# Optimization experiments

Measured on AMD Instinct MI355X. Metric: run time of the kernel, lower is better.

The kernel has to match this reference:

```python
import jax, jax.numpy as jnp
import numpy as np

N_NODES = 100000
N_EDGES = 3200000
D_IN = 96      # sum(latent_dim)
D_OUT = 32     # latent_dim[-1]
N_HEADS = 4
LEAKY_SLOPE = 0.2


def setup_inputs() -> dict:
    key = jax.random.key(0)
    k_x, k_w, k_a, k_src, k_dst = jax.random.split(key, 5)
    x = jax.random.normal(k_x, (N_NODES, D_IN), dtype=jnp.float32)
    # per-head GAT params (xavier-ish scale)
    W = jax.random.normal(k_w, (N_HEADS, D_IN, D_OUT), dtype=jnp.float32) * (1.414 / np.sqrt(D_IN))
    a = jax.random.normal(k_a, (N_HEADS, 2 * D_OUT), dtype=jnp.float32) * 0.1
    edge_src = jax.random.randint(k_src, (N_EDGES,), 0, N_NODES)
    edge_dst = jax.random.randint(k_dst, (N_EDGES,), 0, N_NODES)
    return {"x": x, "W": W, "a": a, "edge_src": edge_src, "edge_dst": edge_dst}


def reference(x, W, a, edge_src, edge_dst):
    # Multi-head sparse GAT layer (SpGraphAttentionLayer, concat=True, eval mode).
    N = x.shape[0]
    n_heads, _, d_out = W.shape
    outs = []
    for i in range(n_heads):  # small fixed head loop; data dims fully vectorized
        h = x @ W[i]                                   # [N, d_out]
        # a @ cat(h[src], h[dst]) == h[src]@a1 + h[dst]@a2 (avoids [E, 2*d_out] concat)
        s = h[edge_src] @ a[i, :d_out] + h[edge_dst] @ a[i, d_out:]   # [E]
        edge_e = jnp.exp(-jax.nn.leaky_relu(s, LEAKY_SLOPE))          # [E]
        # sparse_coo(edge, edge_e, [N,N]) @ h  ==  scatter-add of edge_e * h[dst] into src
        msg = edge_e[:, None] * h[edge_dst]                           # [E, d_out]
        h_prime = jax.ops.segment_sum(msg, edge_src, num_segments=N)  # [N, d_out]
        outs.append(jax.nn.elu(h_prime))
    return jnp.concatenate(outs, axis=1)  # [N, n_heads * d_out]
```

## Files before the change

kernel.cpp:

```cpp
#include <hip/hip_runtime.h>
#include <hip/hip_bf16.h>

#define DIN 96
#define DOUT 32
#define NH 4
#define DTOT 128
#define SLOPE 0.2f
#define NPB 16
#define BSH 7
#define BNODES 128
#define MAXB 1024
#define EPB 16384

__device__ __forceinline__ unsigned int packbf2(float lo, float hi) {
    unsigned int a = __float_as_uint(lo), b = __float_as_uint(hi);
    a += 0x7fffu + ((a >> 16) & 1u);
    b += 0x7fffu + ((b >> 16) & 1u);
    return (a >> 16) | (b & 0xffff0000u);
}

__global__ __launch_bounds__(256) void feat_kernel(
    const float* __restrict__ x, const float* __restrict__ W,
    const float* __restrict__ a,
    unsigned int* __restrict__ hq,
    float2* __restrict__ usrc, float2* __restrict__ vdst,
    int n_nodes)
{
    __shared__ float Wl[DIN * DTOT];
    __shared__ float xs[NPB * DIN];
    __shared__ float al[NH * 2 * DOUT];
    const int t = threadIdx.x;

    for (int i = t; i < DIN * DTOT; i += 256) {
        int k = i >> 7, c = i & 127;
        int head = c >> 5, j = c & 31;
        Wl[i] = W[head * (DIN * DOUT) + k * DOUT + j];
    }
    for (int i = t; i < NH * 2 * DOUT; i += 256) al[i] = a[i];

    const int node0 = blockIdx.x * NPB;
    for (int i = t; i < NPB * DIN; i += 256) {
        int gidx = node0 * DIN + i;
        xs[i] = (gidx < n_nodes * DIN) ? x[gidx] : 0.f;
    }
    __syncthreads();

    const int node = t >> 4;
    const int cb = (t & 15) << 3;
    float acc[8];
#pragma unroll
    for (int j = 0; j < 8; ++j) acc[j] = 0.f;

#pragma unroll 4
    for (int k = 0; k < DIN; ++k) {
        float xv = xs[node * DIN + k];
#pragma unroll
        for (int j = 0; j < 8; ++j)
            acc[j] += xv * Wl[k * DTOT + cb + j];
    }

    const int g = node0 + node;
    if (g < n_nodes) {
        uint4 pk;
        pk.x = packbf2(acc[0], acc[1]);
        pk.y = packbf2(acc[2], acc[3]);
        pk.z = packbf2(acc[4], acc[5]);
        pk.w = packbf2(acc[6], acc[7]);
        *(uint4*)&hq[(size_t)g * 64 + (cb >> 1)] = pk;
    }

    const int head = cb >> 5;
    const int j0 = cb & 31;
    float ps = 0.f, pd = 0.f;
#pragma unroll
    for (int j = 0; j < 8; ++j) {
        ps += acc[j] * al[head * 64 + j0 + j];
        pd += acc[j] * al[head * 64 + 32 + j0 + j];
    }
    ps += __shfl_xor(ps, 1); ps += __shfl_xor(ps, 2);
    pd += __shfl_xor(pd, 1); pd += __shfl_xor(pd, 2);
    if ((t & 3) == 0 && g < n_nodes) {
        usrc[g * NH + head] = make_float2(__expf(-ps), __expf(-SLOPE * ps));
        vdst[g * NH + head] = make_float2(__expf(-pd), __expf(-SLOPE * pd));
    }
}


__global__ __launch_bounds__(256) void bincount_kernel(
    const int* __restrict__ esrc, int* __restrict__ counts, int n_edges, int nb)
{
    __shared__ int bc[MAXB];
    const int t = threadIdx.x;
    for (int i = t; i < nb; i += 256) bc[i] = 0;
    __syncthreads();
    const int base = blockIdx.x * EPB;
    const int end = min(base + EPB, n_edges);
    for (int e = base + t; e < end; e += 256)
        atomicAdd(&bc[esrc[e] >> BSH], 1);
    __syncthreads();
    for (int i = t; i < nb; i += 256)
        if (bc[i] > 0) atomicAdd(&counts[i], bc[i]);
}

__global__ __launch_bounds__(1024) void bscan_kernel(
    const int* __restrict__ counts, int* __restrict__ bbase,
    int* __restrict__ gcur, int* __restrict__ sbase, int nb)
{
    __shared__ int tmp[1024];
    const int t = threadIdx.x;
    int v = (t < nb) ? counts[t] : 0;
    tmp[t] = v;
    __syncthreads();
    for (int off = 1; off < 1024; off <<= 1) {
        int xv = (t >= off) ? tmp[t - off] : 0;
        __syncthreads();
        tmp[t] += xv;
        __syncthreads();
    }
    if (t < nb) {
        int excl = tmp[t] - v;
        bbase[t] = excl;
        gcur[t] = excl;
        sbase[t] = ((excl + 3) & ~3) + t * (4 * BNODES);
    }
}

__global__ __launch_bounds__(256) void binscatter_kernel(
    const int* __restrict__ esrc, const int* __restrict__ edst,
    int* __restrict__ gcur, unsigned int* __restrict__ binned,
    int n_edges, int nb)
{
    __shared__ int bc[MAXB];
    const int t = threadIdx.x;
    for (int i = t; i < nb; i += 256) bc[i] = 0;
    __syncthreads();
    const int base = blockIdx.x * EPB;
    const int end = min(base + EPB, n_edges);
    for (int e = base + t; e < end; e += 256)
        atomicAdd(&bc[esrc[e] >> BSH], 1);
    __syncthreads();
    for (int i = t; i < nb; i += 256) {
        int c = bc[i];
        bc[i] = (c > 0) ? atomicAdd(&gcur[i], c) : 0;
    }
    __syncthreads();
    for (int e = base + t; e < end; e += 256) {
        int s = esrc[e];
        int pos = atomicAdd(&bc[s >> BSH], 1);
        binned[pos] = ((unsigned int)(s & (BNODES - 1)) << 17) | (unsigned int)edst[e];
    }
}

__global__ __launch_bounds__(256) void binfine_kernel(
    const unsigned int* __restrict__ binned,
    const int* __restrict__ counts, const int* __restrict__ bbase,
    const int* __restrict__ sbase,
    int* __restrict__ offs, int* __restrict__ deg,
    int* __restrict__ slots, int n_nodes)
{
    __shared__ int dcnt[BNODES];
    __shared__ int sc[BNODES];
    __shared__ int dcur[BNODES];
    const int t = threadIdx.x;
    const int b = blockIdx.x;
    const int cnt = counts[b];
    const int start = bbase[b];
    const int sb = sbase[b];
    const int node0 = b << BSH;

    if (t < BNODES) dcnt[t] = 0;
    __syncthreads();
    for (int i = t; i < cnt; i += 256)
        atomicAdd(&dcnt[binned[start + i] >> 17], 1);
    __syncthreads();
    int pd = 0;
    if (t < BNODES) { pd = (dcnt[t] + 3) & ~3; sc[t] = pd; }
    __syncthreads();
    for (int off = 1; off < BNODES; off <<= 1) {
        int v = 0;
        if (t < BNODES && t >= off) v = sc[t - off];
        __syncthreads();
        if (t < BNODES) sc[t] += v;
        __syncthreads();
    }
    if (t < BNODES) {
        int o = sb + sc[t] - pd;
        dcur[t] = o;
        int node = node0 + t;
        if (node < n_nodes) { offs[node] = o; deg[node] = dcnt[t]; }
    }
    __syncthreads();
    for (int i = t; i < cnt; i += 256) {
        unsigned int w = binned[start + i];
        int pos = atomicAdd(&dcur[w >> 17], 1);
        slots[pos] = (int)(w & 0x1ffffu);
    }
}

__global__ __launch_bounds__(256) void gather_kernel(
    const int* __restrict__ slots, const int* __restrict__ offsets,
    const int* __restrict__ deg,
    const unsigned int* __restrict__ hv,
    const float2* __restrict__ usrc, const float2* __restrict__ vdst,
    float* __restrict__ out, int n_nodes)
{
    const int t = threadIdx.x;
    const int node = blockIdx.x * 4 + (t >> 6);
    if (node >= n_nodes) return;
    const int l = t & 63;
    const int head = l >> 4;
    const unsigned loff = (unsigned)l << 2;
    const unsigned hoff = (unsigned)head << 3;
    const char* __restrict__ hvb = (const char*)hv;
    const char* __restrict__ vdb = (const char*)vdst;
    const float2 u = usrc[(unsigned)node * 4u + head];
    const int beg = offsets[node];
    const int d = deg[node];

    float ax0 = 0.f, ay0 = 0.f, ax1 = 0.f, ay1 = 0.f;
    float ax2 = 0.f, ay2 = 0.f, ax3 = 0.f, ay3 = 0.f;

#define LDV(c) (*(const float2*)(vdb + ((((unsigned)(c)) << 5) + hoff)))
#define LDW(c) (*(const unsigned int*)(hvb + ((((unsigned)(c)) << 8) + loff)))
#define COMP(vv, ww, AX, AY) do {                                   \
        float e_ = fminf(u.x * (vv).x, u.y * (vv).y);               \
        AX = fmaf(e_, __uint_as_float((ww) << 16), AX);             \
        AY = fmaf(e_, __uint_as_float((ww) & 0xffff0000u), AY);     \
    } while (0)

    int k = 0;
    if (d >= 4) {
        int4 cA = *(const int4*)(slots + beg);
        float2 vA0 = LDV(cA.x), vA1 = LDV(cA.y), vA2 = LDV(cA.z), vA3 = LDV(cA.w);
        unsigned wA0 = LDW(cA.x), wA1 = LDW(cA.y), wA2 = LDW(cA.z), wA3 = LDW(cA.w);

        for (; k + 12 <= d; k += 8) {
            int4 cB = *(const int4*)(slots + beg + k + 4);
            float2 vB0 = LDV(cB.x), vB1 = LDV(cB.y), vB2 = LDV(cB.z), vB3 = LDV(cB.w);
            unsigned wB0 = LDW(cB.x), wB1 = LDW(cB.y), wB2 = LDW(cB.z), wB3 = LDW(cB.w);
            COMP(vA0, wA0, ax0, ay0); COMP(vA1, wA1, ax1, ay1);
            COMP(vA2, wA2, ax2, ay2); COMP(vA3, wA3, ax3, ay3);
            int4 cN = *(const int4*)(slots + beg + k + 8);
            vA0 = LDV(cN.x); vA1 = LDV(cN.y); vA2 = LDV(cN.z); vA3 = LDV(cN.w);
            wA0 = LDW(cN.x); wA1 = LDW(cN.y); wA2 = LDW(cN.z); wA3 = LDW(cN.w);
            COMP(vB0, wB0, ax0, ay0); COMP(vB1, wB1, ax1, ay1);
            COMP(vB2, wB2, ax2, ay2); COMP(vB3, wB3, ax3, ay3);
        }
        if (k + 8 <= d) {
            int4 cB = *(const int4*)(slots + beg + k + 4);
            float2 vB0 = LDV(cB.x), vB1 = LDV(cB.y), vB2 = LDV(cB.z), vB3 = LDV(cB.w);
            unsigned wB0 = LDW(cB.x), wB1 = LDW(cB.y), wB2 = LDW(cB.z), wB3 = LDW(cB.w);
            COMP(vA0, wA0, ax0, ay0); COMP(vA1, wA1, ax1, ay1);
            COMP(vA2, wA2, ax2, ay2); COMP(vA3, wA3, ax3, ay3);
            COMP(vB0, wB0, ax0, ay0); COMP(vB1, wB1, ax1, ay1);
            COMP(vB2, wB2, ax2, ay2); COMP(vB3, wB3, ax3, ay3);
            k += 8;
        } else {
            COMP(vA0, wA0, ax0, ay0); COMP(vA1, wA1, ax1, ay1);
            COMP(vA2, wA2, ax2, ay2); COMP(vA3, wA3, ax3, ay3);
            k += 4;
        }
    }
    for (; k < d; ++k) {
        int c = slots[beg + k];
        float2 v = LDV(c);
        unsigned w = LDW(c);
        COMP(v, w, ax0, ay0);
    }
#undef LDV
#undef LDW
#undef COMP

    float rx = (ax0 + ax1) + (ax2 + ax3);
    float ry = (ay0 + ay1) + (ay2 + ay3);
    rx = rx > 0.f ? rx : __expf(rx) - 1.f;
    ry = ry > 0.f ? ry : __expf(ry) - 1.f;
    ((float2*)out)[(unsigned)node * 64u + l] = make_float2(rx, ry);
}

extern "C" void kernel_launch(void* const* d_in, const int* in_sizes, int n_in,
                              void* d_out, int out_size, void* d_ws, size_t ws_size,
                              hipStream_t stream)
{
    const float* x  = (const float*)d_in[0];
    const float* W  = (const float*)d_in[1];
    const float* a  = (const float*)d_in[2];
    const int* esrc = (const int*)d_in[3];
    const int* edst = (const int*)d_in[4];
    const int n_nodes = in_sizes[0] / DIN;
    const int n_edges = in_sizes[3];
    float* out = (float*)d_out;

    const int nb = (n_nodes + BNODES - 1) >> BSH;

    unsigned int* hq = (unsigned int*)d_ws;
    float2* usrc = (float2*)(hq + (size_t)n_nodes * 64);
    float2* vdst = usrc + (size_t)n_nodes * NH;
    int* offs   = (int*)(vdst + (size_t)n_nodes * NH);
    int* deg    = offs + n_nodes;
    int* counts = deg + n_nodes;
    int* bbase  = counts + MAXB;
    int* gcur   = bbase + MAXB;
    int* sbase  = gcur + MAXB;
    unsigned int* binned = (unsigned int*)(sbase + MAXB);
    int* slots  = (int*)(binned + n_edges);

    hipMemsetAsync(counts, 0, MAXB * sizeof(int), stream);

    feat_kernel<<<(n_nodes + NPB - 1) / NPB, 256, 0, stream>>>(
        x, W, a, hq, usrc, vdst, n_nodes);

    const int binblocks = (n_edges + EPB - 1) / EPB;
    bincount_kernel<<<binblocks, 256, 0, stream>>>(esrc, counts, n_edges, nb);
    bscan_kernel<<<1, 1024, 0, stream>>>(counts, bbase, gcur, sbase, nb);
    binscatter_kernel<<<binblocks, 256, 0, stream>>>(
        esrc, edst, gcur, binned, n_edges, nb);
    binfine_kernel<<<nb, 256, 0, stream>>>(
        binned, counts, bbase, sbase, offs, deg, slots, n_nodes);

    gather_kernel<<<(n_nodes + 3) / 4, 256, 0, stream>>>(
        slots, offs, deg, hq, usrc, vdst, out, n_nodes);
}
```

Before: 501.0 us.

## Register-tile feature GEMM over four nodes and fold counts memset into it

The feature kernel now computes four nodes per thread with 64 nodes per block, reading x directly from global memory as float4 and W from shared memory as split float4 halves. This amortises the per-block W staging over more nodes and cuts shared-memory traffic per FMA. The separate memset of the bin counts is removed; block 0 of the feature kernel zeroes them instead, saving one launch. In exchange each thread holds more registers, and the grid has a quarter as many blocks.

```diff
diff --git a/kernel.cpp b/kernel.cpp
--- a/kernel.cpp
+++ b/kernel.cpp
@@ -6,7 +6,7 @@
 #define NH 4
 #define DTOT 128
 #define SLOPE 0.2f
-#define NPB 16
+#define NPBF 64
 #define BSH 7
 #define BNODES 128
 #define MAXB 1024
@@ -24,64 +24,97 @@
     const float* __restrict__ a,
     unsigned int* __restrict__ hq,
     float2* __restrict__ usrc, float2* __restrict__ vdst,
-    int n_nodes)
-{
-    __shared__ float Wl[DIN * DTOT];
-    __shared__ float xs[NPB * DIN];
+    int* __restrict__ counts, int n_nodes)
+{
+    __shared__ float Wlo[DIN * 64];
+    __shared__ float Whi[DIN * 64];
     __shared__ float al[NH * 2 * DOUT];
     const int t = threadIdx.x;
+
+    if (blockIdx.x == 0)
+        for (int i = t; i < MAXB; i += 256) counts[i] = 0;
 
     for (int i = t; i < DIN * DTOT; i += 256) {
         int k = i >> 7, c = i & 127;
         int head = c >> 5, j = c & 31;
-        Wl[i] = W[head * (DIN * DOUT) + k * DOUT + j];
+        float w = W[head * (DIN * DOUT) + k * DOUT + j];
+        int cbi = c >> 3, jj = c & 7;
+        if (jj < 4) Wlo[(k << 6) + (cbi << 2) + jj] = w;
+        else        Whi[(k << 6) + (cbi << 2) + (jj - 4)] = w;
     }
     for (int i = t; i < NH * 2 * DOUT; i += 256) al[i] = a[i];
-
-    const int node0 = blockIdx.x * NPB;
-    for (int i = t; i < NPB * DIN; i += 256) {
-        int gidx = node0 * DIN + i;
-        xs[i] = (gidx < n_nodes * DIN) ? x[gidx] : 0.f;
-    }
-    __syncthreads();
-
-    const int node = t >> 4;
-    const int cb = (t & 15) << 3;
-    float acc[8];
-#pragma unroll
-    for (int j = 0; j < 8; ++j) acc[j] = 0.f;
-
-#pragma unroll 4
-    for (int k = 0; k < DIN; ++k) {
-        float xv = xs[node * DIN + k];
-#pragma unroll
-        for (int j = 0; j < 8; ++j)
-            acc[j] += xv * Wl[k * DTOT + cb + j];
-    }
-
-    const int g = node0 + node;
-    if (g < n_nodes) {
-        uint4 pk;
-        pk.x = packbf2(acc[0], acc[1]);
-        pk.y = packbf2(acc[2], acc[3]);
-        pk.z = packbf2(acc[4], acc[5]);
-        pk.w = packbf2(acc[6], acc[7]);
-        *(uint4*)&hq[(size_t)g * 64 + (cb >> 1)] = pk;
-    }
-
-    const int head = cb >> 5;
-    const int j0 = cb & 31;
-    float ps = 0.f, pd = 0.f;
-#pragma unroll
-    for (int j = 0; j < 8; ++j) {
-        ps += acc[j] * al[head * 64 + j0 + j];
-        pd += acc[j] * al[head * 64 + 32 + j0 + j];
-    }
-    ps += __shfl_xor(ps, 1); ps += __shfl_xor(ps, 2);
-    pd += __shfl_xor(pd, 1); pd += __shfl_xor(pd, 2);
-    if ((t & 3) == 0 && g < n_nodes) {
-        usrc[g * NH + head] = make_float2(__expf(-ps), __expf(-SLOPE * ps));
-        vdst[g * NH + head] = make_float2(__expf(-pd), __expf(-SLOPE * pd));
+    __syncthreads();
+
+    const int cbi = t & 15;
+    const int ng = t >> 4;
+    const int node0 = blockIdx.x * NPBF;
+    const int g0 = node0 + ng * 4;
+
+    bool ok[4];
+    const float* xp[4];
+#pragma unroll
+    for (int i = 0; i < 4; ++i) {
+        ok[i] = (g0 + i) < n_nodes;
+        xp[i] = x + (size_t)(g0 + i) * DIN;
+    }
+
+    float acc[4][8];
+#pragma unroll
+    for (int i = 0; i < 4; ++i)
+#pragma unroll
+        for (int j = 0; j < 8; ++j) acc[i][j] = 0.f;
+
+    for (int k = 0; k < DIN; k += 4) {
+        float4 xv[4];
+#pragma unroll
+        for (int i = 0; i < 4; ++i)
+            xv[i] = ok[i] ? *(const float4*)(xp[i] + k)
+                          : make_float4(0.f, 0.f, 0.f, 0.f);
+#pragma unroll
+        for (int kk = 0; kk < 4; ++kk) {
+            const float4 wlo = *(const float4*)&Wlo[((k + kk) << 6) + (cbi << 2)];
+            const float4 whi = *(const float4*)&Whi[((k + kk) << 6) + (cbi << 2)];
+#pragma unroll
+            for (int i = 0; i < 4; ++i) {
+                const float xvv = (kk == 0) ? xv[i].x : (kk == 1) ? xv[i].y
+                                 : (kk == 2) ? xv[i].z : xv[i].w;
+                acc[i][0] = fmaf(xvv, wlo.x, acc[i][0]);
+                acc[i][1] = fmaf(xvv, wlo.y, acc[i][1]);
+                acc[i][2] = fmaf(xvv, wlo.z, acc[i][2]);
+                acc[i][3] = fmaf(xvv, wlo.w, acc[i][3]);
+                acc[i][4] = fmaf(xvv, whi.x, acc[i][4]);
+                acc[i][5] = fmaf(xvv, whi.y, acc[i][5]);
+                acc[i][6] = fmaf(xvv, whi.z, acc[i][6]);
+                acc[i][7] = fmaf(xvv, whi.w, acc[i][7]);
+            }
+        }
+    }
+
+    const int head = cbi >> 2;
+    const int j0 = (cbi & 3) << 3;
+#pragma unroll
+    for (int i = 0; i < 4; ++i) {
+        float ps = 0.f, pd = 0.f;
+#pragma unroll
+        for (int j = 0; j < 8; ++j) {
+            ps += acc[i][j] * al[head * 64 + j0 + j];
+            pd += acc[i][j] * al[head * 64 + 32 + j0 + j];
+        }
+        ps += __shfl_xor(ps, 1); ps += __shfl_xor(ps, 2);
+        pd += __shfl_xor(pd, 1); pd += __shfl_xor(pd, 2);
+        const int g = g0 + i;
+        if (ok[i]) {
+            uint4 pk;
+            pk.x = packbf2(acc[i][0], acc[i][1]);
+            pk.y = packbf2(acc[i][2], acc[i][3]);
+            pk.z = packbf2(acc[i][4], acc[i][5]);
+            pk.w = packbf2(acc[i][6], acc[i][7]);
+            *(uint4*)&hq[(size_t)g * 64 + (cbi << 2)] = pk;
+            if ((cbi & 3) == 0) {
+                usrc[g * NH + head] = make_float2(__expf(-ps), __expf(-SLOPE * ps));
+                vdst[g * NH + head] = make_float2(__expf(-pd), __expf(-SLOPE * pd));
+            }
+        }
     }
 }
 
@@ -305,10 +338,8 @@
     unsigned int* binned = (unsigned int*)(sbase + MAXB);
     int* slots  = (int*)(binned + n_edges);
 
-    hipMemsetAsync(counts, 0, MAXB * sizeof(int), stream);
-
-    feat_kernel<<<(n_nodes + NPB - 1) / NPB, 256, 0, stream>>>(
-        x, W, a, hq, usrc, vdst, n_nodes);
+    feat_kernel<<<(n_nodes + NPBF - 1) / NPBF, 256, 0, stream>>>(
+        x, W, a, hq, usrc, vdst, counts, n_nodes);
 
     const int binblocks = (n_edges + EPB - 1) / EPB;
     bincount_kernel<<<binblocks, 256, 0, stream>>>(esrc, counts, n_edges, nb);
```

Result: no change. 495.4 us (-1.1%).
